# Optimization experiments

Measured on AMD Instinct MI355X. Metric: run time of the kernel, lower is better.

## Reference

```python
import jax, jax.numpy as jnp
import numpy as np

B, T, C, H = 4, 4096, 1024, 64

def setup_inputs() -> dict:
    key = jax.random.key(0)
    kx, kq, kk, kv = jax.random.split(key, 4)
    # nn.Linear weights are [out, in]; we store them that way and use einsum.
    s = 1.0 / np.sqrt(C)
    return {
        "x": jax.random.normal(kx, (B, T, C), dtype=jnp.float32),
        "Wq": jax.random.uniform(kq, (H, C), dtype=jnp.float32, minval=-s, maxval=s),
        "Wk": jax.random.uniform(kk, (H, C), dtype=jnp.float32, minval=-s, maxval=s),
        "Wv": jax.random.uniform(kv, (H, C), dtype=jnp.float32, minval=-s, maxval=s),
    }

def reference(x, Wq, Wk, Wv):
    # x: [B, T, C]; W*: [H, C] (torch Linear layout)
    Q = jnp.einsum('btc,hc->bth', x, Wq)  # [B, T, H]
    K = jnp.einsum('btc,hc->bth', x, Wk)
    V = jnp.einsum('btc,hc->bth', x, Wv)
    scale = K.shape[-1] ** -0.5
    scores = jnp.einsum('bqh,bkh->bqk', Q, K) * scale  # [B, T, T]
    Tn = x.shape[1]
    causal = jnp.tril(jnp.ones((Tn, Tn), dtype=bool))
    scores = jnp.where(causal, scores, -jnp.inf)
    attn = jax.nn.softmax(scores, axis=-1)
    return jnp.einsum('bqk,bkh->bqh', attn, V)  # [B, T, H]
```

## Files before the change

kernel.cpp:

```cpp
#include <hip/hip_runtime.h>
#include <hip/hip_bf16.h>

#define B_ 4
#define T_ 4096
#define C_ 1024
#define H_ 64

typedef __bf16 bf16x8 __attribute__((ext_vector_type(8)));
typedef float f32x4 __attribute__((ext_vector_type(4)));
typedef unsigned short u16x8 __attribute__((ext_vector_type(8)));

union Frag8 { uint4 u; bf16x8 b; u16x8 s; };

__device__ inline unsigned short bfbits(float f) {
  union { __hip_bfloat16 h; unsigned short u; } cv;
  cv.h = __float2bfloat16(f);
  return cv.u;
}

__device__ inline float b2f(unsigned u) {
  union { unsigned i; float f; } c; c.i = u << 16; return c.f;
}

__device__ inline bf16x8 ldb8(const unsigned short* p) {
  Frag8 f; f.u = *(const uint4*)p; return f.b;
}

__device__ inline bf16x8 asbf(uint4 u) { Frag8 f; f.u = u; return f.b; }

__device__ inline unsigned pkbf(float a, float b) {
  union { float f; unsigned u; } ua, ub; ua.f = a; ub.f = b;
  return __builtin_amdgcn_perm(ub.u + 0x8000u, ua.u + 0x8000u, 0x07060302u);
}

__device__ inline Frag8 packA(float4 a0, float4 a1) {
  Frag8 af;
  af.s[0] = bfbits(a0.x); af.s[1] = bfbits(a0.y);
  af.s[2] = bfbits(a0.z); af.s[3] = bfbits(a0.w);
  af.s[4] = bfbits(a1.x); af.s[5] = bfbits(a1.y);
  af.s[6] = bfbits(a1.z); af.s[7] = bfbits(a1.w);
  return af;
}

__device__ inline void gload16(const void* g, void* l) {
  __builtin_amdgcn_global_load_lds(
      (const __attribute__((address_space(1))) unsigned int*)g,
      (__attribute__((address_space(3))) unsigned int*)l, 16, 0, 0);
}

__global__ __launch_bounds__(256) void wconv(const float* __restrict__ Wq,
                                             const float* __restrict__ Wk,
                                             const float* __restrict__ Wv,
                                             unsigned short* __restrict__ Wb) {
  int i = blockIdx.x * 256 + threadIdx.x;
  size_t e = (size_t)i * 4;
  const float* src = (e < 65536) ? (Wq + e)
                   : (e < 131072 ? (Wk + (e - 65536)) : (Wv + (e - 131072)));
  float4 v = *(const float4*)src;
  unsigned long long o =
      (unsigned long long)bfbits(v.x)
    | ((unsigned long long)bfbits(v.y) << 16)
    | ((unsigned long long)bfbits(v.z) << 32)
    | ((unsigned long long)bfbits(v.w) << 48);
  *(unsigned long long*)(Wb + e) = o;
}

__global__ __launch_bounds__(256) void qkv_proj(const float* __restrict__ x,
                                                const unsigned short* __restrict__ Wb,
                                                unsigned short* __restrict__ qkv,
                                                unsigned short* __restrict__ Vt) {
  __shared__ float xs[2][2048];
  __shared__ unsigned short Wsh[2][12288];
  const int lane = threadIdx.x & 63;
  const int wave = threadIdx.x >> 6;
  const int q16 = lane & 15, quad = lane >> 4;
  const int x7 = q16 & 7;
  const size_t row0 = (size_t)blockIdx.x * 32;

  const int sr = lane >> 4;
  const int sc_pos = lane & 15;
  const int rloc = lane >> 3;
  const int cpos = lane & 7;

  f32x4 acc[2][3] = {};

  auto stage = [&](int buf, int kc) {
#pragma unroll
    for (int ii = 0; ii < 2; ++ii) {
      int i = wave * 2 + ii;
      int r = i * 4 + sr;
      int sg = (sc_pos >> 1) ^ (r & 7);
      const float* gp = x + (row0 + r) * C_ + kc + sg * 8 + (sc_pos & 1) * 4;
      gload16(gp, &xs[buf][i * 256]);
    }
#pragma unroll
    for (int jj = 0; jj < 6; ++jj) {
      int j = wave * 6 + jj;
      int g = j * 8 + rloc;
      const unsigned short* gp = Wb + (size_t)(g >> 6) * 65536
                                    + (size_t)(g & 63) * C_ + kc + (cpos ^ rloc) * 8;
      gload16(gp, &Wsh[buf][j * 512]);
    }
  };

  stage(0, 0);
  __syncthreads();

  int cur = 0;
  for (int t = 0; t < 16; ++t) {
    if (t < 15) stage(cur ^ 1, (t + 1) * 64);
    const float* Xc = xs[cur];
    const unsigned short* Wc = Wsh[cur];
#pragma unroll
    for (int s = 0; s < 2; ++s) {
      bf16x8 bf[3];
#pragma unroll
      for (int ct = 0; ct < 3; ++ct) {
        int g = wave * 48 + ct * 16 + q16;
        bf[ct] = ldb8(&Wc[g * 64 + (((s * 4 + quad) ^ x7) * 8)]);
      }
#pragma unroll
      for (int rt = 0; rt < 2; ++rt) {
        int r = rt * 16 + q16;
        int p = ((s * 4 + quad) ^ (r & 7)) * 8;
        const float* ap = &Xc[r * 64 + p];
        float4 a0 = *(const float4*)ap;
        float4 a1 = *(const float4*)(ap + 4);
        Frag8 af = packA(a0, a1);
#pragma unroll
        for (int ct = 0; ct < 3; ++ct)
          acc[rt][ct] = __builtin_amdgcn_mfma_f32_16x16x32_bf16(
              af.b, bf[ct], acc[rt][ct], 0, 0, 0);
      }
    }
    __syncthreads();
    cur ^= 1;
  }

  const int bb = (int)(blockIdx.x >> 7);
#pragma unroll
  for (int rt = 0; rt < 2; ++rt) {
    const int t0 = (int)(row0 - (size_t)bb * T_) + rt * 16 + quad * 4;
#pragma unroll
    for (int ct = 0; ct < 3; ++ct) {
      int gcol = wave * 48 + ct * 16;
      int mat = gcol >> 6, h = (gcol & 63) + q16;
      if (mat == 2) {
        ushort4 v;
        v.x = bfbits(acc[rt][ct][0]); v.y = bfbits(acc[rt][ct][1]);
        v.z = bfbits(acc[rt][ct][2]); v.w = bfbits(acc[rt][ct][3]);
        *(ushort4*)(Vt + ((size_t)bb * H_ + h) * T_ + t0) = v;
      } else {
        float scale = (mat == 0) ? 0.18033688f : 1.0f;
#pragma unroll
        for (int r = 0; r < 4; ++r) {
          size_t row = row0 + rt * 16 + quad * 4 + r;
          qkv[(size_t)mat * 1048576 + row * H_ + h] = bfbits(acc[rt][ct][r] * scale);
        }
      }
    }
  }
}

__global__ __launch_bounds__(256) void attn(const unsigned short* __restrict__ Q,
                                            const unsigned short* __restrict__ K,
                                            const unsigned short* __restrict__ Vt,
                                            float* __restrict__ part) {
  const int b = blockIdx.x >> 6;
  const int qblk = 63 - (blockIdx.x & 63);
  const int ki = qblk + 1;
  const int c = blockIdx.y;
  const int c8 = c * 8;
  if (c8 >= ki) return;
  const int kend = (ki < c8 + 8) ? ki : c8 + 8;

  __shared__ unsigned short Ks[2][4096];
  __shared__ unsigned short Vs[2][4096];
  const int lane = threadIdx.x & 63;
  const int wave = threadIdx.x >> 6;
  const int q16 = lane & 15, quad = lane >> 4;
  const int x7 = q16 & 7;
  const int rloc = lane >> 3, cpos = lane & 7;

  const unsigned short* Qb = Q + (size_t)b * T_ * H_;
  const unsigned short* Kb = K + (size_t)b * T_ * H_;
  const unsigned short* Vtb = Vt + (size_t)b * H_ * T_;

  auto stage = [&](int buf, int kt) {
    const int kkb = kt * 64;
#pragma unroll
    for (int ii = 0; ii < 2; ++ii) {
      int i = wave * 2 + ii;
      gload16(Kb + (size_t)(kkb + i * 8 + rloc) * H_ + (cpos ^ rloc) * 8,
              &Ks[buf][i * 512]);
      gload16(Vtb + (size_t)(i * 8 + rloc) * T_ + kkb + (cpos ^ rloc) * 8,
              &Vs[buf][i * 512]);
    }
  };

  const int q0w = qblk * 64 + wave * 16;
  bf16x8 qf0 = ldb8(Qb + (size_t)(q0w + q16) * H_ + quad * 8);
  bf16x8 qf1 = ldb8(Qb + (size_t)(q0w + q16) * H_ + 32 + quad * 8);

  f32x4 o0 = {0.f, 0.f, 0.f, 0.f}, o1 = o0, o2 = o0, o3 = o0;
  float m = -3.0e38f, l = 0.0f;
  const int q_abs = q0w + q16;
  const int src0 = q16 + 32 * (quad & 1);
  const int kbsel = quad >> 1;

  stage(0, c8);
  __syncthreads();

  int cur = 0;
  for (int kt = c8; kt < kend; ++kt) {
    const int kkb = kt * 64;
    if (kt + 1 < kend) stage(cur ^ 1, kt + 1);
    const unsigned short* Kc = Ks[cur];
    const unsigned short* Vc = Vs[cur];

    f32x4 st[4];
#pragma unroll
    for (int kb = 0; kb < 4; ++kb) {
      bf16x8 ka0 = ldb8(&Kc[(kb * 16 + q16) * 64 + ((quad ^ x7) * 8)]);
      bf16x8 ka1 = ldb8(&Kc[(kb * 16 + q16) * 64 + (((quad + 4) ^ x7) * 8)]);
      f32x4 s = {0.f, 0.f, 0.f, 0.f};
      s = __builtin_amdgcn_mfma_f32_16x16x32_bf16(ka0, qf0, s, 0, 0, 0);
      s = __builtin_amdgcn_mfma_f32_16x16x32_bf16(ka1, qf1, s, 0, 0, 0);
      st[kb] = s;
    }
    if (kt == ki - 1) {
#pragma unroll
      for (int kb = 0; kb < 4; ++kb)
#pragma unroll
        for (int r = 0; r < 4; ++r)
          if (kkb + kb * 16 + quad * 4 + r > q_abs) st[kb][r] = -3.0e38f;
    }

    float mloc = fmaxf(fmaxf(st[0][0], st[0][1]), fmaxf(st[0][2], st[0][3]));
#pragma unroll
    for (int kb = 1; kb < 4; ++kb)
      mloc = fmaxf(mloc, fmaxf(fmaxf(st[kb][0], st[kb][1]), fmaxf(st[kb][2], st[kb][3])));
    mloc = fmaxf(mloc, __shfl_xor(mloc, 16));
    mloc = fmaxf(mloc, __shfl_xor(mloc, 32));
    float mnew = fmaxf(m, mloc);
    float alpha = exp2f(m - mnew);
    float lsum = 0.f;
    unsigned pk[4][2];
#pragma unroll
    for (int kb = 0; kb < 4; ++kb) {
      float p0 = exp2f(st[kb][0] - mnew);
      float p1 = exp2f(st[kb][1] - mnew);
      float p2 = exp2f(st[kb][2] - mnew);
      float p3 = exp2f(st[kb][3] - mnew);
      lsum += (p0 + p1) + (p2 + p3);
      pk[kb][0] = pkbf(p0, p1);
      pk[kb][1] = pkbf(p2, p3);
    }
    lsum += __shfl_xor(lsum, 16);
    lsum += __shfl_xor(lsum, 32);
    l = l * alpha + lsum;
    m = mnew;
    float ar0 = __shfl(alpha, quad * 4 + 0);
    float ar1 = __shfl(alpha, quad * 4 + 1);
    float ar2 = __shfl(alpha, quad * 4 + 2);
    float ar3 = __shfl(alpha, quad * 4 + 3);
    o0[0] *= ar0; o0[1] *= ar1; o0[2] *= ar2; o0[3] *= ar3;
    o1[0] *= ar0; o1[1] *= ar1; o1[2] *= ar2; o1[3] *= ar3;
    o2[0] *= ar0; o2[1] *= ar1; o2[2] *= ar2; o2[3] *= ar3;
    o3[0] *= ar0; o3[1] *= ar1; o3[2] *= ar2; o3[3] *= ar3;

#pragma unroll
    for (int kb2 = 0; kb2 < 2; ++kb2) {
      int xA = __shfl((int)pk[2 * kb2][0], src0);
      int xB = __shfl((int)pk[2 * kb2 + 1][0], src0);
      int yA = __shfl((int)pk[2 * kb2][1], src0);
      int yB = __shfl((int)pk[2 * kb2 + 1][1], src0);
      int zA = __shfl((int)pk[2 * kb2][0], src0 + 16);
      int zB = __shfl((int)pk[2 * kb2 + 1][0], src0 + 16);
      int wA = __shfl((int)pk[2 * kb2][1], src0 + 16);
      int wB = __shfl((int)pk[2 * kb2 + 1][1], src0 + 16);
      Frag8 pf;
      pf.u.x = (unsigned)(kbsel ? xB : xA);
      pf.u.y = (unsigned)(kbsel ? yB : yA);
      pf.u.z = (unsigned)(kbsel ? zB : zA);
      pf.u.w = (unsigned)(kbsel ? wB : wA);
      int vp = ((kb2 * 4 + quad) ^ x7) * 8;
      bf16x8 v0 = ldb8(&Vc[(q16 + 0)  * 64 + vp]);
      bf16x8 v1 = ldb8(&Vc[(q16 + 16) * 64 + vp]);
      bf16x8 v2 = ldb8(&Vc[(q16 + 32) * 64 + vp]);
      bf16x8 v3 = ldb8(&Vc[(q16 + 48) * 64 + vp]);
      o0 = __builtin_amdgcn_mfma_f32_16x16x32_bf16(pf.b, v0, o0, 0, 0, 0);
      o1 = __builtin_amdgcn_mfma_f32_16x16x32_bf16(pf.b, v1, o1, 0, 0, 0);
      o2 = __builtin_amdgcn_mfma_f32_16x16x32_bf16(pf.b, v2, o2, 0, 0, 0);
      o3 = __builtin_amdgcn_mfma_f32_16x16x32_bf16(pf.b, v3, o3, 0, 0, 0);
    }
    __syncthreads();
    cur ^= 1;
  }

  const int qtl = qblk * 4 + wave;
  float* Pf = part + ((size_t)((b << 8) + qtl) * 8 + c) * 544;
  unsigned* Pw = (unsigned*)Pf;
  Pw[0 * 64 + lane] = pkbf(o0[0], o0[1]);
  Pw[1 * 64 + lane] = pkbf(o0[2], o0[3]);
  Pw[2 * 64 + lane] = pkbf(o1[0], o1[1]);
  Pw[3 * 64 + lane] = pkbf(o1[2], o1[3]);
  Pw[4 * 64 + lane] = pkbf(o2[0], o2[1]);
  Pw[5 * 64 + lane] = pkbf(o2[2], o2[3]);
  Pw[6 * 64 + lane] = pkbf(o3[0], o3[1]);
  Pw[7 * 64 + lane] = pkbf(o3[2], o3[3]);
  if (quad == 0) { Pf[512 + q16] = m; Pf[528 + q16] = l; }
}

__global__ __launch_bounds__(256) void attn_merge(const float* __restrict__ part,
                                                  float* __restrict__ out) {
  const int qt = blockIdx.x;
  const int qtl = qt & 255, b = qt >> 8;
  const int ki = (qtl >> 2) + 1;
  const int nch = (ki + 7) >> 3;
  const int t = threadIdx.x;
  const int row = t >> 4, col0 = (t & 15) * 4;
  const int i = (col0 >> 4) * 4 + (row & 3);
  const int lane0 = (row >> 2) * 16 + (col0 & 15);
  const int sh = 16 * (i & 1);
  const float* P0 = part + (size_t)qt * 8 * 544;
  float M = -3.0e38f;
  for (int c2 = 0; c2 < nch; ++c2) M = fmaxf(M, P0[c2 * 544 + 512 + row]);
  float L = 0.f;
  float ax = 0.f, ay = 0.f, az = 0.f, aw = 0.f;
  for (int c2 = 0; c2 < nch; ++c2) {
    const float* P = P0 + c2 * 544;
    float w = exp2f(P[512 + row] - M);
    L += w * P[528 + row];
    const unsigned* Pw = (const unsigned*)P;
    uint4 wd = *(const uint4*)&Pw[(i >> 1) * 64 + lane0];
    ax += w * b2f((wd.x >> sh) & 0xffffu);
    ay += w * b2f((wd.y >> sh) & 0xffffu);
    az += w * b2f((wd.z >> sh) & 0xffffu);
    aw += w * b2f((wd.w >> sh) & 0xffffu);
  }
  float inv = 1.0f / L;
  float4 r = {ax * inv, ay * inv, az * inv, aw * inv};
  *(float4*)(out + ((size_t)b * T_ + qtl * 16 + row) * H_ + col0) = r;
}

extern "C" void kernel_launch(void* const* d_in, const int* in_sizes, int n_in,
                              void* d_out, int out_size, void* d_ws, size_t ws_size,
                              hipStream_t stream) {
  const float* x  = (const float*)d_in[0];
  const float* Wq = (const float*)d_in[1];
  const float* Wk = (const float*)d_in[2];
  const float* Wv = (const float*)d_in[3];
  float* out = (float*)d_out;
  unsigned short* ws = (unsigned short*)d_ws;

  unsigned short* Wb  = ws;
  unsigned short* qkv = ws + 196608;
  unsigned short* Vt  = qkv + (size_t)2 * 1048576;
  float* part = (float*)(ws + 196608 + (size_t)3 * 1048576);

  wconv<<<192, 256, 0, stream>>>(Wq, Wk, Wv, Wb);
  qkv_proj<<<512, 256, 0, stream>>>(x, Wb, qkv, Vt);
  attn<<<dim3(256, 8), 256, 0, stream>>>(qkv, qkv + 1048576, Vt, part);
  attn_merge<<<1024, 256, 0, stream>>>(part, out);
}
```

Measured before the change: 161.6 us.

## Halve attention split chunk size and defer online-softmax rescaling

The attention kernel's key-chunk size becomes a runtime parameter. When the workspace is large enough, it is halved from 8 to 4 key tiles, which doubles the grid's y-dimension to 16 splits and raises parallelism for the causal workload. The merge kernel is adjusted to read the variable number of partial slots. Separately, the online softmax skips updating the running max and rescaling the accumulators whenever every lane's new local max is within 8 (log2 units) of the current max. This removes the exp and shuffle/multiply work on most iterations, at the cost of some bf16 range headroom and more partial-result traffic for the merge.

```diff
diff --git a/kernel.cpp b/kernel.cpp
--- a/kernel.cpp
+++ b/kernel.cpp
@@ -165,14 +165,16 @@
 __global__ __launch_bounds__(256) void attn(const unsigned short* __restrict__ Q,
                                             const unsigned short* __restrict__ K,
                                             const unsigned short* __restrict__ Vt,
-                                            float* __restrict__ part) {
+                                            float* __restrict__ part,
+                                            int lgch, int nslots) {
   const int b = blockIdx.x >> 6;
   const int qblk = 63 - (blockIdx.x & 63);
   const int ki = qblk + 1;
   const int c = blockIdx.y;
-  const int c8 = c * 8;
-  if (c8 >= ki) return;
-  const int kend = (ki < c8 + 8) ? ki : c8 + 8;
+  const int cst = c << lgch;
+  if (cst >= ki) return;
+  const int tcnt = 1 << lgch;
+  const int kend = (ki < cst + tcnt) ? ki : cst + tcnt;
 
   __shared__ unsigned short Ks[2][4096];
   __shared__ unsigned short Vs[2][4096];
@@ -208,11 +210,11 @@
   const int src0 = q16 + 32 * (quad & 1);
   const int kbsel = quad >> 1;
 
-  stage(0, c8);
+  stage(0, cst);
   __syncthreads();
 
   int cur = 0;
-  for (int kt = c8; kt < kend; ++kt) {
+  for (int kt = cst; kt < kend; ++kt) {
     const int kkb = kt * 64;
     if (kt + 1 < kend) stage(cur ^ 1, kt + 1);
     const unsigned short* Kc = Ks[cur];
@@ -242,8 +244,8 @@
       mloc = fmaxf(mloc, fmaxf(fmaxf(st[kb][0], st[kb][1]), fmaxf(st[kb][2], st[kb][3])));
     mloc = fmaxf(mloc, __shfl_xor(mloc, 16));
     mloc = fmaxf(mloc, __shfl_xor(mloc, 32));
-    float mnew = fmaxf(m, mloc);
-    float alpha = exp2f(m - mnew);
+    const bool defer = __all(mloc - m <= 8.0f);
+    const float mnew = defer ? m : fmaxf(m, mloc);
     float lsum = 0.f;
     unsigned pk[4][2];
 #pragma unroll
@@ -258,16 +260,21 @@
     }
     lsum += __shfl_xor(lsum, 16);
     lsum += __shfl_xor(lsum, 32);
-    l = l * alpha + lsum;
-    m = mnew;
-    float ar0 = __shfl(alpha, quad * 4 + 0);
-    float ar1 = __shfl(alpha, quad * 4 + 1);
-    float ar2 = __shfl(alpha, quad * 4 + 2);
-    float ar3 = __shfl(alpha, quad * 4 + 3);
-    o0[0] *= ar0; o0[1] *= ar1; o0[2] *= ar2; o0[3] *= ar3;
-    o1[0] *= ar0; o1[1] *= ar1; o1[2] *= ar2; o1[3] *= ar3;
-    o2[0] *= ar0; o2[1] *= ar1; o2[2] *= ar2; o2[3] *= ar3;
-    o3[0] *= ar0; o3[1] *= ar1; o3[2] *= ar2; o3[3] *= ar3;
+    if (defer) {
+      l += lsum;
+    } else {
+      float alpha = exp2f(m - mnew);
+      l = l * alpha + lsum;
+      m = mnew;
+      float ar0 = __shfl(alpha, quad * 4 + 0);
+      float ar1 = __shfl(alpha, quad * 4 + 1);
+      float ar2 = __shfl(alpha, quad * 4 + 2);
+      float ar3 = __shfl(alpha, quad * 4 + 3);
+      o0[0] *= ar0; o0[1] *= ar1; o0[2] *= ar2; o0[3] *= ar3;
+      o1[0] *= ar0; o1[1] *= ar1; o1[2] *= ar2; o1[3] *= ar3;
+      o2[0] *= ar0; o2[1] *= ar1; o2[2] *= ar2; o2[3] *= ar3;
+      o3[0] *= ar0; o3[1] *= ar1; o3[2] *= ar2; o3[3] *= ar3;
+    }
 
 #pragma unroll
     for (int kb2 = 0; kb2 < 2; ++kb2) {
@@ -299,7 +306,7 @@
   }
 
   const int qtl = qblk * 4 + wave;
-  float* Pf = part + ((size_t)((b << 8) + qtl) * 8 + c) * 544;
+  float* Pf = part + ((size_t)((b << 8) + qtl) * nslots + c) * 544;
   unsigned* Pw = (unsigned*)Pf;
   Pw[0 * 64 + lane] = pkbf(o0[0], o0[1]);
   Pw[1 * 64 + lane] = pkbf(o0[2], o0[3]);
@@ -313,17 +320,18 @@
 }
 
 __global__ __launch_bounds__(256) void attn_merge(const float* __restrict__ part,
-                                                  float* __restrict__ out) {
+                                                  float* __restrict__ out,
+                                                  int lgch, int nslots) {
   const int qt = blockIdx.x;
   const int qtl = qt & 255, b = qt >> 8;
   const int ki = (qtl >> 2) + 1;
-  const int nch = (ki + 7) >> 3;
+  const int nch = (ki + (1 << lgch) - 1) >> lgch;
   const int t = threadIdx.x;
   const int row = t >> 4, col0 = (t & 15) * 4;
   const int i = (col0 >> 4) * 4 + (row & 3);
   const int lane0 = (row >> 2) * 16 + (col0 & 15);
   const int sh = 16 * (i & 1);
-  const float* P0 = part + (size_t)qt * 8 * 544;
+  const float* P0 = part + (size_t)qt * nslots * 544;
   float M = -3.0e38f;
   for (int c2 = 0; c2 < nch; ++c2) M = fmaxf(M, P0[c2 * 544 + 512 + row]);
   float L = 0.f;
@@ -359,8 +367,13 @@
   unsigned short* Vt  = qkv + (size_t)2 * 1048576;
   float* part = (float*)(ws + 196608 + (size_t)3 * 1048576);
 
+  const size_t base_bytes = ((size_t)196608 + (size_t)3 * 1048576) * 2;
+  const size_t need16 = base_bytes + (size_t)1024 * 16 * 544 * 4;
+  int lgch = 3, ny = 8, nslots = 8;
+  if (ws_size >= need16) { lgch = 2; ny = 16; nslots = 16; }
+
   wconv<<<192, 256, 0, stream>>>(Wq, Wk, Wv, Wb);
   qkv_proj<<<512, 256, 0, stream>>>(x, Wb, qkv, Vt);
-  attn<<<dim3(256, 8), 256, 0, stream>>>(qkv, qkv + 1048576, Vt, part);
-  attn_merge<<<1024, 256, 0, stream>>>(part, out);
-}
+  attn<<<dim3(256, ny), 256, 0, stream>>>(qkv, qkv + 1048576, Vt, part, lgch, nslots);
+  attn_merge<<<1024, 256, 0, stream>>>(part, out, lgch, nslots);
+}
```

New measurement: 162.7 us. No clear change (+0.7%).
